# Kernel tuning notes

Hardware: AMD Instinct MI355X
Metric: run time of the kernel (lower is better)

The kernel has to match this reference:

```python
import jax, jax.numpy as jnp
import numpy as np

B, T, TREF, NBINS, H = 4096, 8192, 8192, 50, 32  # np.linspace(lo,hi,50) -> 49 bins
EPS = 1e-10


def setup_inputs() -> dict:
    key = jax.random.key(0)
    k0, k1, k2, k3, k4, k5 = jax.random.split(key, 6)
    return {
        "current_returns": jax.random.normal(k0, (B, T), jnp.float32) * 0.02,
        "reference_returns": jax.random.normal(k1, (TREF,), jnp.float32) * 0.02,
        "w1": jax.random.normal(k2, (H, 1), jnp.float32) * 0.5,   # Linear(1, H).weight
        "b1": jax.random.normal(k3, (H,), jnp.float32) * 0.1,
        "w2": jax.random.normal(k4, (H, H), jnp.float32) * 0.1,   # Linear(H, H).weight
        "b2": jax.random.normal(k5, (H,), jnp.float32) * 0.1,
    }


def _kl_from_hists(ref, curr, ref_min, ref_max):
    # Faithful to InformationTheory.kl_divergence with n_bins=50 (49 equal-width bins).
    nb = NBINS - 1
    lo = jnp.minimum(ref_min, curr.min())
    hi = jnp.maximum(ref_max, curr.max())
    width = (hi - lo) / nb

    def hist_density(x):
        # np.histogram(x, bins=linspace(lo,hi,50), density=True); all x in [lo,hi],
        # right edge goes to last bin (handled by clip).
        idx = jnp.clip(jnp.floor((x - lo) / width).astype(jnp.int32), 0, nb - 1)
        counts = jnp.zeros(nb, jnp.float32).at[idx].add(1.0)
        return counts / (x.shape[0] * width)

    p = hist_density(ref) + EPS
    q = hist_density(curr) + EPS
    p = p / p.sum()
    q = q / q.sum()
    return jnp.sum(p * jnp.log(p / q))


def reference(current_returns, reference_returns, w1, b1, w2, b2):
    ref = reference_returns
    ref_min, ref_max = ref.min(), ref.max()
    kl = jax.vmap(lambda c: _kl_from_hists(ref, c, ref_min, ref_max))(current_returns)  # [B]
    kl = jax.lax.stop_gradient(kl)  # original detaches before building kl_tensor
    x = kl[:, None]                                  # [B, 1]
    h = jax.nn.relu(x @ w1.T + b1)                   # [B, H]
    encoded = h @ w2.T + b2                          # [B, H]
    return kl, encoded
```

## Files before the change

### kernel.cpp

```cpp
#include <hip/hip_runtime.h>
#include <math.h>

constexpr int T_LEN  = 8192;
constexpr int B_ROWS = 4096;
constexpr int NB     = 49;
constexpr int NC     = 32;
constexpr int HDIM   = 32;
constexpr int FBINS  = 8192;
constexpr float EPSF = 1e-10f;

constexpr int WS_CDF_OFF    = 8;
constexpr int WS_BINNED_OFF = 8208;

#define HP(i) ((i) + ((i) >> 5))

__device__ __forceinline__ void sync_lds() {
    asm volatile("s_waitcnt lgkmcnt(0)" ::: "memory");
    __builtin_amdgcn_s_barrier();
    __builtin_amdgcn_sched_barrier(0);
}

__global__ __launch_bounds__(256)
void ref_cdf_kernel(const float* __restrict__ ref, float* __restrict__ wsf) {
    __shared__ float sv[FBINS];
    __shared__ int   hist[HP(FBINS)];
    __shared__ int   wsum[4];
    __shared__ float rmn4[4], rmx4[4];
    const int tid  = threadIdx.x;
    const int lane = tid & 63;
    const int wave = tid >> 6;

    const float4* r4 = (const float4*)ref;
    float4* sv4 = (float4*)sv;
    float mn = 3.0e38f, mx = -3.0e38f;
    #pragma unroll
    for (int i = 0; i < 8; ++i) {
        float4 v = r4[tid + i * 256];
        sv4[tid + i * 256] = v;
        mn = fminf(mn, fminf(fminf(v.x, v.y), fminf(v.z, v.w)));
        mx = fmaxf(mx, fmaxf(fmaxf(v.x, v.y), fmaxf(v.z, v.w)));
    }
    for (int i = tid; i < HP(FBINS); i += 256) hist[i] = 0;
    #pragma unroll
    for (int off = 32; off > 0; off >>= 1) {
        mn = fminf(mn, __shfl_xor(mn, off));
        mx = fmaxf(mx, __shfl_xor(mx, off));
    }
    if (lane == 0) { rmn4[wave] = mn; rmx4[wave] = mx; }
    __syncthreads();
    const float rmin = fminf(fminf(rmn4[0], rmn4[1]), fminf(rmn4[2], rmn4[3]));
    const float rmax = fmaxf(fmaxf(rmx4[0], rmx4[1]), fmaxf(rmx4[2], rmx4[3]));
    const float finv = (float)FBINS / (rmax - rmin);

    for (int i = tid; i < FBINS; i += 256) {
        int fb = min(max((int)((sv[i] - rmin) * finv), 0), FBINS - 1);
        atomicAdd(&hist[HP(fb)], 1);
    }
    __syncthreads();

    const int base = tid * 32;
    int s = 0;
    #pragma unroll
    for (int j = 0; j < 32; ++j) {
        int h = hist[HP(base + j)]; hist[HP(base + j)] = s; s += h;
    }
    const int own = s;
    int incl = s;
    #pragma unroll
    for (int off = 1; off < 64; off <<= 1) {
        int t = __shfl_up(incl, off);
        if (lane >= off) incl += t;
    }
    if (lane == 63) wsum[wave] = incl;
    __syncthreads();
    int woff = 0;
    #pragma unroll
    for (int w = 0; w < 4; ++w) if (w < wave) woff += wsum[w];
    const int add = woff + incl - own;
    #pragma unroll
    for (int j = 0; j < 32; ++j) hist[HP(base + j)] += add;
    __syncthreads();

    int* cdf = (int*)(wsf + WS_CDF_OFF);
    for (int i = tid; i < FBINS; i += 256) cdf[i] = hist[HP(i)];
    if (tid == 0) { cdf[FBINS] = T_LEN; wsf[0] = rmin; wsf[1] = rmax; }
    __syncthreads();

    float* binned = wsf + WS_BINNED_OFF;
    for (int i = tid; i < FBINS; i += 256) {
        float x = sv[i];
        int fb = min(max((int)((x - rmin) * finv), 0), FBINS - 1);
        int pos = atomicAdd(&hist[HP(fb)], 1);
        binned[pos] = x;
    }
}

__global__ __launch_bounds__(256, 4)
void kl_lds_kernel(const float* __restrict__ cur,
                   const float* __restrict__ wsf,
                   const float* __restrict__ w1,
                   const float* __restrict__ b1,
                   const float* __restrict__ w2,
                   const float* __restrict__ b2,
                   float* __restrict__ kl_out,
                   float* __restrict__ enc_out) {
    __shared__ float row[T_LEN];
    __shared__ unsigned hq[NC * NB];
    __shared__ float rmnS[4], rmxS[4];

    const int tid  = threadIdx.x;
    const int lane = tid & 63;
    const int wave = tid >> 6;
    const int b    = blockIdx.x;
    const float* src = cur + (size_t)b * T_LEN;

    #pragma unroll
    for (int i = 0; i < 8; ++i) {
        const float* g = src + wave * 2048 + i * 256 + lane * 4;
        __builtin_amdgcn_global_load_lds(
            (const __attribute__((address_space(1))) void*)g,
            (__attribute__((address_space(3))) void*)&row[wave * 2048 + i * 256],
            16, 0, 0);
    }
    for (int i = tid; i < NC * NB; i += 256) hq[i] = 0u;
    const float rmin = wsf[0], rmax = wsf[1];
    __syncthreads();

    const float4* row4 = (const float4*)row;
    float mn = 3.0e38f, mx = -3.0e38f;
    #pragma unroll
    for (int i = 0; i < 8; ++i) {
        float4 t = row4[tid + i * 256];
        mn = fminf(mn, fminf(fminf(t.x, t.y), fminf(t.z, t.w)));
        mx = fmaxf(mx, fmaxf(fmaxf(t.x, t.y), fmaxf(t.z, t.w)));
    }
    #pragma unroll
    for (int off = 32; off > 0; off >>= 1) {
        mn = fminf(mn, __shfl_xor(mn, off));
        mx = fmaxf(mx, __shfl_xor(mx, off));
    }
    if (lane == 0) { rmnS[wave] = mn; rmxS[wave] = mx; }
    sync_lds();

    const float lo = fminf(rmin,
        fminf(fminf(rmnS[0], rmnS[1]), fminf(rmnS[2], rmnS[3])));
    const float hi = fmaxf(rmax,
        fmaxf(fmaxf(rmxS[0], rmxS[1]), fmaxf(rmxS[2], rmxS[3])));
    const float width = (hi - lo) / (float)NB;
    const float winv = 1.0f / width, nlw = -lo * winv;

    unsigned* myq = hq + (tid & (NC - 1)) * NB;
    #pragma unroll
    for (int i = 0; i < 8; ++i) {
        float4 t = row4[tid + i * 256];
        int i0 = min((int)fmaf(t.x, winv, nlw), NB - 1);
        int i1 = min((int)fmaf(t.y, winv, nlw), NB - 1);
        int i2 = min((int)fmaf(t.z, winv, nlw), NB - 1);
        int i3 = min((int)fmaf(t.w, winv, nlw), NB - 1);
        atomicAdd(&myq[i0], 1u); atomicAdd(&myq[i1], 1u);
        atomicAdd(&myq[i2], 1u); atomicAdd(&myq[i3], 1u);
    }
    sync_lds();

    if (tid < 64) {
        const bool act = lane < NB;
        const float inv = 1.0f / ((float)T_LEN * width);
        float p = 0.0f, q = 0.0f;
        if (act) {
            unsigned sq = 0u;
            #pragma unroll
            for (int c = 0; c < NC; ++c) sq += hq[c * NB + lane];
            q = (float)sq * inv + EPSF;
        }
        int C = T_LEN;
        if (lane < NB - 1) {
            const float kp1  = (float)(lane + 1);
            const float finv = (float)FBINS / (rmax - rmin);
            const int* cdf = (const int*)(wsf + WS_CDF_OFF);
            const float* binned = wsf + WS_BINNED_OFF;
            const float t = fmaf(width, kp1, lo);
            int fb = (int)floorf((t - rmin) * finv);
            int a  = min(max(fb - 2, 0), FBINS);
            int bb = min(max(fb + 3, 0), FBINS);
            int ia = cdf[a], ib = cdf[bb];
            C = ia;
            for (int i = ia; i < ib; i += 4) {
                float x0 = binned[i];
                float x1 = (i + 1 < ib) ? binned[i + 1] : 3.0e38f;
                float x2 = (i + 2 < ib) ? binned[i + 2] : 3.0e38f;
                float x3 = (i + 3 < ib) ? binned[i + 3] : 3.0e38f;
                C += ((x0 - lo) / width < kp1) ? 1 : 0;
                C += ((x1 - lo) / width < kp1) ? 1 : 0;
                C += ((x2 - lo) / width < kp1) ? 1 : 0;
                C += ((x3 - lo) / width < kp1) ? 1 : 0;
            }
        }
        int Cprev = __shfl_up(C, 1);
        if (lane == 0) Cprev = 0;
        if (act) p = (float)(C - Cprev) * inv + EPSF;

        float P = p, Q = q;
        #pragma unroll
        for (int off = 32; off > 0; off >>= 1) {
            P += __shfl_xor(P, off);
            Q += __shfl_xor(Q, off);
        }
        float term = 0.0f;
        if (act) {
            const float pn = p / P;
            const float qn = q / Q;
            term = pn * logf(pn / qn);
        }
        #pragma unroll
        for (int off = 32; off > 0; off >>= 1) term += __shfl_xor(term, off);
        if (lane == 0) kl_out[b] = term;

        if (lane < HDIM) {
            float acc = b2[lane];
            #pragma unroll
            for (int t2 = 0; t2 < HDIM; ++t2) {
                float h = fmaxf(fmaf(term, w1[t2], b1[t2]), 0.0f);
                acc = fmaf(h, w2[lane * HDIM + t2], acc);
            }
            enc_out[(size_t)b * HDIM + lane] = acc;
        }
    }
}

extern "C" void kernel_launch(void* const* d_in, const int* in_sizes, int n_in,
                              void* d_out, int out_size, void* d_ws, size_t ws_size,
                              hipStream_t stream) {
    const float* cur = (const float*)d_in[0];
    const float* ref = (const float*)d_in[1];
    const float* w1  = (const float*)d_in[2];
    const float* b1  = (const float*)d_in[3];
    const float* w2  = (const float*)d_in[4];
    const float* b2  = (const float*)d_in[5];
    float* out = (float*)d_out;
    float* wsf = (float*)d_ws;

    ref_cdf_kernel<<<1, 256, 0, stream>>>(ref, wsf);
    kl_lds_kernel<<<B_ROWS, 256, 0, stream>>>(
        cur, wsf, w1, b1, w2, b2, out, out + B_ROWS);
}
```

Measured before the change: 47.55 us.

## Process eight rows per block with double-buffered async LDS staging

Each block now handles eight rows instead of one. The next row's global-to-LDS load is issued while the current row is histogrammed, using two LDS row buffers and vmcnt waits. Per-row histograms, lo and width go to a small LDS record, and the reference-CDF/KL/MLP tail then runs once per wave across the eight rows. This is meant to hide load latency and amortize per-block setup. In exchange, LDS use doubles, occupancy drops to two blocks per CU, and rows inside a block run serially with barriers.

```diff
diff --git a/kernel.cpp b/kernel.cpp
--- a/kernel.cpp
+++ b/kernel.cpp
@@ -7,6 +7,8 @@
 constexpr int NC     = 32;
 constexpr int HDIM   = 32;
 constexpr int FBINS  = 8192;
+constexpr int RPB    = 8;
+constexpr int RECW   = 52;
 constexpr float EPSF = 1e-10f;
 
 constexpr int WS_CDF_OFF    = 8;
@@ -95,83 +97,109 @@
     }
 }
 
-__global__ __launch_bounds__(256, 4)
-void kl_lds_kernel(const float* __restrict__ cur,
-                   const float* __restrict__ wsf,
-                   const float* __restrict__ w1,
-                   const float* __restrict__ b1,
-                   const float* __restrict__ w2,
-                   const float* __restrict__ b2,
-                   float* __restrict__ kl_out,
-                   float* __restrict__ enc_out) {
-    __shared__ float row[T_LEN];
+__global__ __launch_bounds__(256, 2)
+void kl_pipe_kernel(const float* __restrict__ cur,
+                    const float* __restrict__ wsf,
+                    const float* __restrict__ w1,
+                    const float* __restrict__ b1,
+                    const float* __restrict__ w2,
+                    const float* __restrict__ b2,
+                    float* __restrict__ kl_out,
+                    float* __restrict__ enc_out) {
+    __shared__ float    buf[2][T_LEN];
     __shared__ unsigned hq[NC * NB];
-    __shared__ float rmnS[4], rmxS[4];
+    __shared__ float    scmn[4], scmx[4];
+    __shared__ float    rec[RPB][RECW];
 
     const int tid  = threadIdx.x;
     const int lane = tid & 63;
     const int wave = tid >> 6;
-    const int b    = blockIdx.x;
-    const float* src = cur + (size_t)b * T_LEN;
-
-    #pragma unroll
-    for (int i = 0; i < 8; ++i) {
-        const float* g = src + wave * 2048 + i * 256 + lane * 4;
-        __builtin_amdgcn_global_load_lds(
-            (const __attribute__((address_space(1))) void*)g,
-            (__attribute__((address_space(3))) void*)&row[wave * 2048 + i * 256],
-            16, 0, 0);
-    }
-    for (int i = tid; i < NC * NB; i += 256) hq[i] = 0u;
+    const int rbase = blockIdx.x * RPB;
+    const float* src = cur + (size_t)rbase * T_LEN;
     const float rmin = wsf[0], rmax = wsf[1];
-    __syncthreads();
-
-    const float4* row4 = (const float4*)row;
-    float mn = 3.0e38f, mx = -3.0e38f;
-    #pragma unroll
-    for (int i = 0; i < 8; ++i) {
-        float4 t = row4[tid + i * 256];
-        mn = fminf(mn, fminf(fminf(t.x, t.y), fminf(t.z, t.w)));
-        mx = fmaxf(mx, fmaxf(fmaxf(t.x, t.y), fmaxf(t.z, t.w)));
-    }
-    #pragma unroll
-    for (int off = 32; off > 0; off >>= 1) {
-        mn = fminf(mn, __shfl_xor(mn, off));
-        mx = fmaxf(mx, __shfl_xor(mx, off));
-    }
-    if (lane == 0) { rmnS[wave] = mn; rmxS[wave] = mx; }
-    sync_lds();
-
-    const float lo = fminf(rmin,
-        fminf(fminf(rmnS[0], rmnS[1]), fminf(rmnS[2], rmnS[3])));
-    const float hi = fmaxf(rmax,
-        fmaxf(fmaxf(rmxS[0], rmxS[1]), fmaxf(rmxS[2], rmxS[3])));
-    const float width = (hi - lo) / (float)NB;
-    const float winv = 1.0f / width, nlw = -lo * winv;
-
-    unsigned* myq = hq + (tid & (NC - 1)) * NB;
-    #pragma unroll
-    for (int i = 0; i < 8; ++i) {
-        float4 t = row4[tid + i * 256];
-        int i0 = min((int)fmaf(t.x, winv, nlw), NB - 1);
-        int i1 = min((int)fmaf(t.y, winv, nlw), NB - 1);
-        int i2 = min((int)fmaf(t.z, winv, nlw), NB - 1);
-        int i3 = min((int)fmaf(t.w, winv, nlw), NB - 1);
-        atomicAdd(&myq[i0], 1u); atomicAdd(&myq[i1], 1u);
-        atomicAdd(&myq[i2], 1u); atomicAdd(&myq[i3], 1u);
-    }
-    sync_lds();
-
-    if (tid < 64) {
+
+    auto stage = [&](int r, int pbuf) {
+        const float* g = src + (size_t)r * T_LEN + wave * 2048;
+        #pragma unroll
+        for (int i = 0; i < 8; ++i) {
+            __builtin_amdgcn_global_load_lds(
+                (const __attribute__((address_space(1))) void*)(g + i * 256 + lane * 4),
+                (__attribute__((address_space(3))) void*)&buf[pbuf][wave * 2048 + i * 256],
+                16, 0, 0);
+        }
+    };
+
+    stage(0, 0);
+
+    #pragma unroll
+    for (int r = 0; r < RPB; ++r) {
+        if (r + 1 < RPB) stage(r + 1, (r + 1) & 1);
+
+        for (int i = tid; i < NC * NB; i += 256) hq[i] = 0u;
+
+        if (r + 1 < RPB) {
+            asm volatile("s_waitcnt vmcnt(8)" ::: "memory");
+        } else {
+            asm volatile("s_waitcnt vmcnt(0)" ::: "memory");
+        }
+        __builtin_amdgcn_sched_barrier(0);
+
+        const float4* b4 = (const float4*)buf[r & 1];
+        float4 v[8];
+        #pragma unroll
+        for (int i = 0; i < 8; ++i) v[i] = b4[wave * 512 + i * 64 + lane];
+
+        float mn = 3.0e38f, mx = -3.0e38f;
+        #pragma unroll
+        for (int i = 0; i < 8; ++i) {
+            mn = fminf(mn, fminf(fminf(v[i].x, v[i].y), fminf(v[i].z, v[i].w)));
+            mx = fmaxf(mx, fmaxf(fmaxf(v[i].x, v[i].y), fmaxf(v[i].z, v[i].w)));
+        }
+        #pragma unroll
+        for (int off = 32; off > 0; off >>= 1) {
+            mn = fminf(mn, __shfl_xor(mn, off));
+            mx = fmaxf(mx, __shfl_xor(mx, off));
+        }
+        if (lane == 0) { scmn[wave] = mn; scmx[wave] = mx; }
+        sync_lds();
+
+        const float lo = fminf(rmin,
+            fminf(fminf(scmn[0], scmn[1]), fminf(scmn[2], scmn[3])));
+        const float hi = fmaxf(rmax,
+            fmaxf(fmaxf(scmx[0], scmx[1]), fmaxf(scmx[2], scmx[3])));
+        const float width = (hi - lo) / (float)NB;
+        const float winv = 1.0f / width, nlw = -lo * winv;
+
+        unsigned* myq = hq + (tid & (NC - 1)) * NB;
+        #pragma unroll
+        for (int i = 0; i < 8; ++i) {
+            int i0 = min((int)fmaf(v[i].x, winv, nlw), NB - 1);
+            int i1 = min((int)fmaf(v[i].y, winv, nlw), NB - 1);
+            int i2 = min((int)fmaf(v[i].z, winv, nlw), NB - 1);
+            int i3 = min((int)fmaf(v[i].w, winv, nlw), NB - 1);
+            atomicAdd(&myq[i0], 1u); atomicAdd(&myq[i1], 1u);
+            atomicAdd(&myq[i2], 1u); atomicAdd(&myq[i3], 1u);
+        }
+        sync_lds();
+
+        if (tid < NB) {
+            unsigned sq = 0u;
+            #pragma unroll
+            for (int c = 0; c < NC; ++c) sq += hq[c * NB + tid];
+            rec[r][tid] = (float)sq;
+        }
+        if (tid == NB)     rec[r][NB]     = lo;
+        if (tid == NB + 1) rec[r][NB + 1] = width;
+        sync_lds();
+    }
+
+    for (int rr = wave; rr < RPB; rr += 4) {
+        const float lo = rec[rr][NB], width = rec[rr][NB + 1];
         const bool act = lane < NB;
         const float inv = 1.0f / ((float)T_LEN * width);
         float p = 0.0f, q = 0.0f;
-        if (act) {
-            unsigned sq = 0u;
-            #pragma unroll
-            for (int c = 0; c < NC; ++c) sq += hq[c * NB + lane];
-            q = (float)sq * inv + EPSF;
-        }
+        if (act) q = rec[rr][lane] * inv + EPSF;
+
         int C = T_LEN;
         if (lane < NB - 1) {
             const float kp1  = (float)(lane + 1);
@@ -213,7 +241,7 @@
         }
         #pragma unroll
         for (int off = 32; off > 0; off >>= 1) term += __shfl_xor(term, off);
-        if (lane == 0) kl_out[b] = term;
+        if (lane == 0) kl_out[rbase + rr] = term;
 
         if (lane < HDIM) {
             float acc = b2[lane];
@@ -222,7 +250,7 @@
                 float h = fmaxf(fmaf(term, w1[t2], b1[t2]), 0.0f);
                 acc = fmaf(h, w2[lane * HDIM + t2], acc);
             }
-            enc_out[(size_t)b * HDIM + lane] = acc;
+            enc_out[(size_t)(rbase + rr) * HDIM + lane] = acc;
         }
     }
 }
@@ -240,6 +268,6 @@
     float* wsf = (float*)d_ws;
 
     ref_cdf_kernel<<<1, 256, 0, stream>>>(ref, wsf);
-    kl_lds_kernel<<<B_ROWS, 256, 0, stream>>>(
+    kl_pipe_kernel<<<B_ROWS / RPB, 256, 0, stream>>>(
         cur, wsf, w1, b1, w2, b2, out, out + B_ROWS);
 }
```

After: 49.98 us. 5.1% more time.
